# Kernel tuning notes

Hardware: AMD Instinct MI355X
Metric: run time of the kernel (lower is better)

## Reference

```python
import jax, jax.numpy as jnp
import numpy as np

GAMMA = 1.0  # matches init_kwargs gamma
B, N, M = 128, 512, 512


def setup_inputs() -> dict:
    key = jax.random.key(0)
    D = jax.random.uniform(key, (B, N, M), dtype=jnp.float32)
    return {"D": D}


def _softmin3(a, b, c, gamma):
    # soft_min over the 3 DP neighbors: -gamma * logsumexp(-x/gamma)
    z = jnp.stack([a, b, c], axis=0) * (-1.0 / gamma)
    return -gamma * jax.nn.logsumexp(z, axis=0)


def reference(D):
    """Soft-DTW forward: returns R[:, N, M], shape (B,).
    DP over rows (lax.scan), inner scan over columns carries R[i, j-1].
    Vectorized over the batch dimension.
    """
    gamma = GAMMA
    b, n, m = D.shape
    dt = D.dtype
    inf = jnp.array(jnp.inf, dt)

    def row_step(prev_row, d_row):
        # prev_row: (b, m+1) = R[i-1, 0..m]; d_row: (b, m) = D[:, i-1, :]
        def col_step(left, xs):
            diag, up, d = xs  # each (b,)
            new = d + _softmin3(diag, up, left, gamma)
            return new, new
        xs = (prev_row[:, :-1].T, prev_row[:, 1:].T, d_row.T)  # each (m, b)
        _, outs = jax.lax.scan(col_step, jnp.full((b,), inf, dt), xs)
        new_row = jnp.concatenate([jnp.full((b, 1), inf, dt), outs.T], axis=1)
        return new_row, None

    # R[0, :] = [0, inf, inf, ...]
    init = jnp.concatenate([jnp.zeros((b, 1), dt), jnp.full((b, m), inf, dt)], axis=1)
    final_row, _ = jax.lax.scan(row_step, init, jnp.swapaxes(D, 0, 1))  # scan over rows (n, b, m)
    return final_row[:, -1]
```

## Files before the change

kernel.cpp:

```cpp
#include <hip/hip_runtime.h>


#define BB 128
#define NN 512
#define MM 512
#define BIGF 1e30f
#define L2E  1.4426950408889634f

template<int P, int U>
__device__ __forceinline__ void dostep(
    const float* __restrict__ Db, int k, int jb,
    float (&r1)[8], float (&r2)[8], float4 (&buf)[2][8][2],
    int& irow, float& sh, float& shprev, float& x0)
{
    {
        const int r = irow < 0 ? 0 : (irow > NN - 1 ? NN - 1 : irow);
        const float4* lp = (const float4*)(Db + ((r << 9) + jb));
        buf[P ^ 1][U][0] = lp[0];
        buf[P ^ 1][U][1] = lp[1];
        irow += 1;
    }

    float nv[8];
    #pragma unroll
    for (int cc = 7; cc >= 0; --cc) {
        const int c = cc;
        float up_, lf, dg;
        up_ = r1[c];
        if (c == 0) {
            lf = (k == 0) ? BIGF : sh;
            dg = (k == 0) ? x0   : shprev;
        } else {
            lf = r1[c - 1];
            dg = r2[c - 1];
        }
        const int par  = (c <= U) ? P : (P ^ 1);
        const int slot = (c <= U) ? (U - c) : (8 + U - c);
        const float4 f4 = buf[par][slot][c >> 2];
        const float d = ((c & 3) == 0) ? f4.x :
                        ((c & 3) == 1) ? f4.y :
                        ((c & 3) == 2) ? f4.z : f4.w;

        const float mn = __builtin_fminf(__builtin_fminf(dg, up_), lf);
        const float md = __builtin_amdgcn_fmed3f(dg, up_, lf);
        const float mx = __builtin_fmaxf(__builtin_fmaxf(dg, up_), lf);
        const float e  = 1.0f + __builtin_amdgcn_exp2f(mn - md)
                              + __builtin_amdgcn_exp2f(mn - mx);
        nv[c] = __builtin_fmaf(d, L2E, mn - __builtin_amdgcn_logf(e));
    }

    x0 = BIGF;
    #pragma unroll
    for (int c = 0; c < 8; ++c) { r2[c] = r1[c]; r1[c] = nv[c]; }
    shprev = sh;
    sh = __shfl_up(r1[7], 1, 64);
}

#define STEP8A(DB) \
    dostep<0,0>(DB,k,jb,r1,r2,buf,irow,sh,shprev,x0); \
    dostep<0,1>(DB,k,jb,r1,r2,buf,irow,sh,shprev,x0); \
    dostep<0,2>(DB,k,jb,r1,r2,buf,irow,sh,shprev,x0); \
    dostep<0,3>(DB,k,jb,r1,r2,buf,irow,sh,shprev,x0); \
    dostep<0,4>(DB,k,jb,r1,r2,buf,irow,sh,shprev,x0); \
    dostep<0,5>(DB,k,jb,r1,r2,buf,irow,sh,shprev,x0); \
    dostep<0,6>(DB,k,jb,r1,r2,buf,irow,sh,shprev,x0); \
    dostep<0,7>(DB,k,jb,r1,r2,buf,irow,sh,shprev,x0);

#define STEP8B(DB) \
    dostep<1,0>(DB,k,jb,r1,r2,buf,irow,sh,shprev,x0); \
    dostep<1,1>(DB,k,jb,r1,r2,buf,irow,sh,shprev,x0); \
    dostep<1,2>(DB,k,jb,r1,r2,buf,irow,sh,shprev,x0); \
    dostep<1,3>(DB,k,jb,r1,r2,buf,irow,sh,shprev,x0); \
    dostep<1,4>(DB,k,jb,r1,r2,buf,irow,sh,shprev,x0); \
    dostep<1,5>(DB,k,jb,r1,r2,buf,irow,sh,shprev,x0); \
    dostep<1,6>(DB,k,jb,r1,r2,buf,irow,sh,shprev,x0); \
    dostep<1,7>(DB,k,jb,r1,r2,buf,irow,sh,shprev,x0);

__launch_bounds__(64, 1)
__global__ void softdtw_wave(const float* __restrict__ D, float* __restrict__ out) {
    const int b = blockIdx.x;
    const int k = threadIdx.x & 63;
    const int jb = k << 3;
    const float* __restrict__ Db = D + (size_t)b * (NN * MM);

    float r1[8], r2[8];
    float4 buf[2][8][2];
    #pragma unroll
    for (int c = 0; c < 8; ++c) { r1[c] = BIGF; r2[c] = BIGF; }
    #pragma unroll
    for (int p = 0; p < 2; ++p)
        #pragma unroll
        for (int w = 0; w < 8; ++w) {
            buf[p][w][0] = make_float4(0.f, 0.f, 0.f, 0.f);
            buf[p][w][1] = make_float4(0.f, 0.f, 0.f, 0.f);
        }

    #pragma unroll
    for (int w = 0; w < 8; ++w) {
        const int i0 = w - jb;
        const int r = i0 < 0 ? 0 : (i0 > NN - 1 ? NN - 1 : i0);
        const float4* lp = (const float4*)(Db + ((r << 9) + jb));
        buf[0][w][0] = lp[0];
        buf[0][w][1] = lp[1];
    }

    int irow = 8 - jb;
    float sh = BIGF, shprev = BIGF, x0 = 0.0f;

    #pragma unroll 1
    for (int qq = 0; qq < 63; ++qq) {
        STEP8A(Db)
        STEP8B(Db)
    }
    STEP8A(Db)
    dostep<1,0>(Db,k,jb,r1,r2,buf,irow,sh,shprev,x0);
    dostep<1,1>(Db,k,jb,r1,r2,buf,irow,sh,shprev,x0);
    dostep<1,2>(Db,k,jb,r1,r2,buf,irow,sh,shprev,x0);
    dostep<1,3>(Db,k,jb,r1,r2,buf,irow,sh,shprev,x0);
    dostep<1,4>(Db,k,jb,r1,r2,buf,irow,sh,shprev,x0);
    dostep<1,5>(Db,k,jb,r1,r2,buf,irow,sh,shprev,x0);
    dostep<1,6>(Db,k,jb,r1,r2,buf,irow,sh,shprev,x0);

    if (k == 63) out[b] = r1[7] * 0.6931471805599453f;
}

extern "C" void kernel_launch(void* const* d_in, const int* in_sizes, int n_in,
                              void* d_out, int out_size, void* d_ws, size_t ws_size,
                              hipStream_t stream) {
    const float* D = (const float*)d_in[0];
    float* out = (float*)d_out;
    softdtw_wave<<<BB, 64, 0, stream>>>(D, out);
}
```

Before: 388.2 us.

## Switch soft-DTW recurrence to linear exp domain with periodic wave-wide renormalization

The recurrence now tracks P = exp(-R) instead of R, so each cell becomes one exp2 of the cost times the sum of its three neighbours. This replaces the min/med/max, two exp2 and one log per cell of the log-sum-exp form. To avoid underflow, every 16 steps the wavefront is rescaled by a power of two taken from the wave-wide maximum, and the exponent is accumulated and folded back in with a final log. Rows past the end are fed a large poison cost. The risk is lost precision or underflow when values along one anti-diagonal span more than the float exponent range.

```diff
diff --git a/kernel.cpp b/kernel.cpp
--- a/kernel.cpp
+++ b/kernel.cpp
@@ -4,56 +4,83 @@
 #define BB 128
 #define NN 512
 #define MM 512
-#define BIGF 1e30f
-#define L2E  1.4426950408889634f
+#define L2E 1.4426950408889634f
+#define LN2 0.6931471805599453f
+#define DPOIS 1.0e4f
 
-template<int P, int U>
+__device__ __forceinline__ int iclamp(int x, int lo, int hi) {
+    return x < lo ? lo : (x > hi ? hi : x);
+}
+
+template<int PAR, int U>
 __device__ __forceinline__ void dostep(
     const float* __restrict__ Db, int k, int jb,
     float (&r1)[8], float (&r2)[8], float4 (&buf)[2][8][2],
     int& irow, float& sh, float& shprev, float& x0)
 {
     {
-        const int r = irow < 0 ? 0 : (irow > NN - 1 ? NN - 1 : irow);
+        const int r = iclamp(irow, 0, NN - 1);
         const float4* lp = (const float4*)(Db + ((r << 9) + jb));
-        buf[P ^ 1][U][0] = lp[0];
-        buf[P ^ 1][U][1] = lp[1];
+        float4 a  = lp[0];
+        float4 b4 = lp[1];
+        if (irow >= NN) {
+            a  = make_float4(DPOIS, DPOIS, DPOIS, DPOIS);
+            b4 = make_float4(DPOIS, DPOIS, DPOIS, DPOIS);
+        }
+        buf[PAR ^ 1][U][0] = a;
+        buf[PAR ^ 1][U][1] = b4;
         irow += 1;
     }
 
     float nv[8];
     #pragma unroll
-    for (int cc = 7; cc >= 0; --cc) {
+    for (int cc = 7; cc >= 1; --cc) {
         const int c = cc;
-        float up_, lf, dg;
-        up_ = r1[c];
-        if (c == 0) {
-            lf = (k == 0) ? BIGF : sh;
-            dg = (k == 0) ? x0   : shprev;
-        } else {
-            lf = r1[c - 1];
-            dg = r2[c - 1];
-        }
-        const int par  = (c <= U) ? P : (P ^ 1);
+        const float up_ = r1[c];
+        const float lf  = r1[c - 1];
+        const float dg  = r2[c - 1];
+        const int par  = (c <= U) ? PAR : (PAR ^ 1);
         const int slot = (c <= U) ? (U - c) : (8 + U - c);
         const float4 f4 = buf[par][slot][c >> 2];
         const float d = ((c & 3) == 0) ? f4.x :
                         ((c & 3) == 1) ? f4.y :
                         ((c & 3) == 2) ? f4.z : f4.w;
-
-        const float mn = __builtin_fminf(__builtin_fminf(dg, up_), lf);
-        const float md = __builtin_amdgcn_fmed3f(dg, up_, lf);
-        const float mx = __builtin_fmaxf(__builtin_fmaxf(dg, up_), lf);
-        const float e  = 1.0f + __builtin_amdgcn_exp2f(mn - md)
-                              + __builtin_amdgcn_exp2f(mn - mx);
-        nv[c] = __builtin_fmaf(d, L2E, mn - __builtin_amdgcn_logf(e));
+        const float w = __builtin_amdgcn_exp2f(-L2E * d);
+        nv[c] = w * ((up_ + lf) + dg);
+    }
+    {
+        const float up_ = r1[0];
+        const float lf  = (k == 0) ? 0.0f : sh;
+        const float dg  = (k == 0) ? x0   : shprev;
+        const float d   = buf[PAR][U][0].x;
+        const float w = __builtin_amdgcn_exp2f(-L2E * d);
+        nv[0] = w * ((up_ + lf) + dg);
     }
 
-    x0 = BIGF;
+    x0 = 0.0f;
     #pragma unroll
     for (int c = 0; c < 8; ++c) { r2[c] = r1[c]; r1[c] = nv[c]; }
     shprev = sh;
     sh = __shfl_up(r1[7], 1, 64);
+}
+
+__device__ __forceinline__ void renorm(float (&r1)[8], float (&r2)[8],
+                                       float& sh, float& shprev, float& gexp)
+{
+    float mx = __builtin_fmaxf(r1[0], r2[0]);
+    #pragma unroll
+    for (int c = 1; c < 8; ++c)
+        mx = __builtin_fmaxf(mx, __builtin_fmaxf(r1[c], r2[c]));
+    #pragma unroll
+    for (int d = 1; d < 64; d <<= 1)
+        mx = __builtin_fmaxf(mx, __shfl_xor(mx, d, 64));
+    const int eb = (__float_as_int(mx) >> 23) & 255;
+    const int ex = (eb > 0 && eb < 255) ? (eb - 127) : 0;
+    const float rs = __int_as_float((127 - ex) << 23);
+    #pragma unroll
+    for (int c = 0; c < 8; ++c) { r1[c] *= rs; r2[c] *= rs; }
+    sh *= rs; shprev *= rs;
+    gexp += (float)ex;
 }
 
 #define STEP8A(DB) \
@@ -86,7 +113,7 @@
     float r1[8], r2[8];
     float4 buf[2][8][2];
     #pragma unroll
-    for (int c = 0; c < 8; ++c) { r1[c] = BIGF; r2[c] = BIGF; }
+    for (int c = 0; c < 8; ++c) { r1[c] = 0.0f; r2[c] = 0.0f; }
     #pragma unroll
     for (int p = 0; p < 2; ++p)
         #pragma unroll
@@ -98,20 +125,24 @@
     #pragma unroll
     for (int w = 0; w < 8; ++w) {
         const int i0 = w - jb;
-        const int r = i0 < 0 ? 0 : (i0 > NN - 1 ? NN - 1 : i0);
+        const int r = iclamp(i0, 0, NN - 1);
         const float4* lp = (const float4*)(Db + ((r << 9) + jb));
         buf[0][w][0] = lp[0];
         buf[0][w][1] = lp[1];
     }
 
     int irow = 8 - jb;
-    float sh = BIGF, shprev = BIGF, x0 = 0.0f;
+    float sh = 0.0f, shprev = 0.0f;
+    float x0 = 1.0f;
+    float gexp = 0.0f;
 
     #pragma unroll 1
     for (int qq = 0; qq < 63; ++qq) {
+        renorm(r1, r2, sh, shprev, gexp);
         STEP8A(Db)
         STEP8B(Db)
     }
+    renorm(r1, r2, sh, shprev, gexp);
     STEP8A(Db)
     dostep<1,0>(Db,k,jb,r1,r2,buf,irow,sh,shprev,x0);
     dostep<1,1>(Db,k,jb,r1,r2,buf,irow,sh,shprev,x0);
@@ -121,7 +152,9 @@
     dostep<1,5>(Db,k,jb,r1,r2,buf,irow,sh,shprev,x0);
     dostep<1,6>(Db,k,jb,r1,r2,buf,irow,sh,shprev,x0);
 
-    if (k == 63) out[b] = r1[7] * 0.6931471805599453f;
+    if (k == 63) {
+        out[b] = -(__builtin_amdgcn_logf(r1[7]) + gexp) * LN2;
+    }
 }
 
 extern "C" void kernel_launch(void* const* d_in, const int* in_sizes, int n_in,
```

New measurement: 461.3 us. 18.8% more time.
